# Optimization experiments

Hardware: AMD Instinct MI355X
Metric: run time of the kernel (lower is better)

The kernel has to match this reference:

```python
import jax, jax.numpy as jnp
import numpy as np

N, D_IN, H, C, K = 16384, 2048, 4096, 256, 256


def setup_inputs() -> dict:
    key = jax.random.key(0)
    ks = jax.random.split(key, 13)

    def lin(kw, kb, fan_in, fan_out):
        # torch Linear default init: U(-1/sqrt(fan_in), 1/sqrt(fan_in)); stored as [in, out]
        bound = 1.0 / np.sqrt(fan_in)
        W = jax.random.uniform(kw, (fan_in, fan_out), jnp.float32, -bound, bound)
        b = jax.random.uniform(kb, (fan_out,), jnp.float32, -bound, bound)
        return W, b

    W_e1, b_e1 = lin(ks[0], ks[1], D_IN, H)
    W_e2, b_e2 = lin(ks[2], ks[3], H, C)
    W_d1, b_d1 = lin(ks[4], ks[5], C, H)
    W_d2, b_d2 = lin(ks[6], ks[7], H, D_IN)
    # codebooks init U(-1/K, 1/K) per the torch code
    cb1 = jax.random.uniform(ks[8], (K, C), jnp.float32, -1.0 / K, 1.0 / K)
    cb2 = jax.random.uniform(ks[9], (K, C), jnp.float32, -1.0 / K, 1.0 / K)
    cb3 = jax.random.uniform(ks[10], (K, C), jnp.float32, -1.0 / K, 1.0 / K)
    x = jax.random.normal(ks[11], (N, D_IN), jnp.float32)
    return {"x": x, "W_e1": W_e1, "b_e1": b_e1, "W_e2": W_e2, "b_e2": b_e2,
            "cb1": cb1, "cb2": cb2, "cb3": cb3,
            "W_d1": W_d1, "b_d1": b_d1, "W_d2": W_d2, "b_d2": b_d2}


def _vq_stage(z, cb):
    # dist[n,k] = sum_c (cb[k,c] - z[n,c])^2 = ||z||^2 - 2 z.cb^T + ||cb||^2
    # (same math as the torch N x K x C broadcast, expressed as a GEMM)
    d = (jnp.sum(z * z, axis=1, keepdims=True)
         - 2.0 * (z @ cb.T)
         + jnp.sum(cb * cb, axis=1))            # [N, K]
    nearest = jnp.argmin(d, axis=1)             # [N]
    zq = cb[nearest]                            # gather [N, C]
    return nearest, zq


def reference(x, W_e1, b_e1, W_e2, b_e2, cb1, cb2, cb3, W_d1, b_d1, W_d2, b_d2):
    ze_1 = jax.nn.relu(x @ W_e1 + b_e1) @ W_e2 + b_e2     # [N, C]
    nearest_1, zq_1 = _vq_stage(ze_1, cb1)
    ze_2 = ze_1 - zq_1
    nearest_2, zq_2 = _vq_stage(ze_2, cb2)
    ze_3 = ze_2 - zq_2
    nearest_3, zq_3 = _vq_stage(ze_3, cb3)
    # straight-through estimator
    decoder_input = ze_1 + jax.lax.stop_gradient(zq_1 + zq_2 + zq_3 - ze_1)
    x_hat = jax.nn.sigmoid(decoder_input @ W_d1 + b_d1) @ W_d2 + b_d2
    return (x_hat, ze_1, ze_2, ze_3, zq_1, zq_2, zq_3, nearest_1, nearest_2, nearest_3)
```

## Files before the change

kernel.cpp:

```cpp
#include <hip/hip_runtime.h>
#include <cstddef>


#define NN 16384
#define DIN 2048
#define HH 4096
#define CC 256
#define QRED ((size_t)4096 * 256)
#define NZ 24

typedef unsigned short ushortT;
typedef __attribute__((ext_vector_type(8))) short bf16x8;
typedef __attribute__((ext_vector_type(4))) float f32x4;

__device__ __forceinline__ ushortT f2b(float v) {
    unsigned int u = __float_as_uint(v);
    return (ushortT)((u + 0x7fffu + ((u >> 16) & 1u)) >> 16);
}
__device__ __forceinline__ float b2f(ushortT s) {
    return __uint_as_float(((unsigned int)s) << 16);
}
__device__ __forceinline__ void split3(float v, ushortT& h, ushortT& m, ushortT& l) {
    h = f2b(v);
    float r1 = v - b2f(h);
    m = f2b(r1);
    l = f2b(r1 - b2f(m));
}

__device__ __forceinline__ void gld16(const void* g, void* l) {
    __builtin_amdgcn_global_load_lds(
        (const __attribute__((address_space(1))) unsigned int*)g,
        (__attribute__((address_space(3))) unsigned int*)l,
        16, 0, 0);
}

template<int NP>
__launch_bounds__(256)
__global__ void tsplit(const float* __restrict__ W,
                       ushortT* __restrict__ T0,
                       ushortT* __restrict__ T1,
                       ushortT* __restrict__ T2,
                       int K, int N)
{
    __shared__ float tile[32][33];
    const int k0 = blockIdx.y * 32, n0 = blockIdx.x * 32;
    const int c = threadIdx.x & 31, r = threadIdx.x >> 5;
    #pragma unroll
    for (int i = 0; i < 4; ++i)
        tile[r + 8*i][c] = W[(size_t)(k0 + r + 8*i) * N + n0 + c];
    __syncthreads();
    #pragma unroll
    for (int i = 0; i < 4; ++i) {
        const int nl = r + 8*i, kl = c;
        float v = tile[kl][nl];
        size_t o = (size_t)(n0 + nl) * K + k0 + kl;
        ushortT h = f2b(v);
        T0[o] = h;
        if (NP > 1) {
            float r1 = v - b2f(h);
            ushortT m = f2b(r1);
            T1[o] = m;
            T2[o] = f2b(r1 - b2f(m));
        }
    }
}

__launch_bounds__(256)
__global__ void split_src(const float* __restrict__ X,
                          ushortT* __restrict__ P0, ushortT* __restrict__ P1,
                          ushortT* __restrict__ P2, size_t n4)
{
    for (size_t i = (size_t)blockIdx.x * 256 + threadIdx.x; i < n4;
         i += (size_t)gridDim.x * 256) {
        float4 v = *(const float4*)(X + i * 4);
        ushort4 hv, mv, lv;
        split3(v.x, ((ushortT*)&hv)[0], ((ushortT*)&mv)[0], ((ushortT*)&lv)[0]);
        split3(v.y, ((ushortT*)&hv)[1], ((ushortT*)&mv)[1], ((ushortT*)&lv)[1]);
        split3(v.z, ((ushortT*)&hv)[2], ((ushortT*)&mv)[2], ((ushortT*)&lv)[2]);
        split3(v.w, ((ushortT*)&hv)[3], ((ushortT*)&mv)[3], ((ushortT*)&lv)[3]);
        *(ushort4*)(P0 + i * 4) = hv;
        *(ushort4*)(P1 + i * 4) = mv;
        *(ushort4*)(P2 + i * 4) = lv;
    }
}

template<int NSEG, int KSH, int NTC, int EPI, int OM>
__launch_bounds__(512, 2)
__global__ void gemm256(const ushortT* __restrict__ Ab, size_t aPl,
                        const ushortT* __restrict__ Bb, size_t bPl,
                        const float* __restrict__ bias,
                        float* __restrict__ Cf,
                        ushortT* __restrict__ Ob, size_t oPl,
                        int N, int K)
{
    __shared__ ushortT sh[65536];

    const int t    = threadIdx.x;
    const int lane = t & 63;
    const int wid  = t >> 6;
    const int l15  = lane & 15;
    const int l4   = lane >> 4;
    const int bm   = blockIdx.y * 256;
    const int bn   = blockIdx.x * 256;
    const int wm   = (wid >> 2) * 128;
    const int wn   = (wid & 3) * 64;
    const int t0   = (OM == 3) ? blockIdx.z * NTC : 0;

    constexpr unsigned PA_PACK = 0x210100u;
    constexpr unsigned PB_PACK = 0x012010u;

    const int trow = t >> 3;
    const unsigned tcol = (unsigned)(((t & 7) ^ (trow & 7)) * 8);
    unsigned gA[4], gB[4];
    #pragma unroll
    for (int i = 0; i < 4; ++i) {
        gA[i] = (unsigned)(bm + i * 64 + trow) * (unsigned)K + tcol;
        gB[i] = (unsigned)(bn + i * 64 + trow) * (unsigned)K + tcol;
    }
    const int ldsT = t * 8;

    auto stageH = [&](int buf, int gtt, int half) {
        const int seg = (NSEG > 1) ? (gtt >> KSH) : 0;
        const unsigned kin = ((unsigned)(gtt & ((1 << KSH) - 1))) << 6;
        const unsigned pa = (NSEG > 1) ? ((PA_PACK >> (seg * 4)) & 15u) : 0u;
        const unsigned pb = (NSEG > 1) ? ((PB_PACK >> (seg * 4)) & 15u) : 0u;
        const ushortT* Abase = Ab + (size_t)pa * aPl + kin;
        const ushortT* Bbase = Bb + (size_t)pb * bPl + kin;
        ushortT* lb = sh + buf * 32768;
        if (half == 0) {
            gld16(Abase + gA[0], lb + 0 * 4096 + ldsT);
            gld16(Abase + gA[2], lb + 2 * 4096 + ldsT);
            gld16(Bbase + gB[0], lb + 16384 + 0 * 4096 + ldsT);
            gld16(Bbase + gB[1], lb + 16384 + 1 * 4096 + ldsT);
        } else {
            gld16(Bbase + gB[2], lb + 16384 + 2 * 4096 + ldsT);
            gld16(Bbase + gB[3], lb + 16384 + 3 * 4096 + ldsT);
            gld16(Abase + gA[1], lb + 1 * 4096 + ldsT);
            gld16(Abase + gA[3], lb + 3 * 4096 + ldsT);
        }
    };

    f32x4 acc[8][4] = {};

    stageH(0, t0, 0);
    stageH(0, t0, 1);

    #pragma unroll 1
    for (int tt = 0; tt < NTC; ++tt) {
        const int buf = tt & 1;
        const ushortT* As = sh + buf * 32768;
        const ushortT* Bs = As + 16384;
        const bool notlast = (tt + 1 < NTC);
        bf16x8 a_[4], b_[4];

        asm volatile("s_waitcnt vmcnt(2)" ::: "memory");
        __builtin_amdgcn_sched_barrier(0);
        __builtin_amdgcn_s_barrier();
        __builtin_amdgcn_sched_barrier(0);
        #pragma unroll
        for (int ni = 0; ni < 4; ++ni) {
            const int rb = wn + ni * 16 + l15;
            b_[ni] = *(const bf16x8*)&Bs[rb * 64 + (l4 ^ (rb & 7)) * 8];
        }
        #pragma unroll
        for (int mi = 0; mi < 4; ++mi) {
            const int ra = wm + mi * 16 + l15;
            a_[mi] = *(const bf16x8*)&As[ra * 64 + (l4 ^ (ra & 7)) * 8];
        }
        if (notlast) stageH(buf ^ 1, t0 + tt + 1, 0);
        asm volatile("s_waitcnt lgkmcnt(0)" ::: "memory");
        __builtin_amdgcn_sched_barrier(0);
        __builtin_amdgcn_s_setprio(1);
        #pragma unroll
        for (int mi = 0; mi < 4; ++mi)
            #pragma unroll
            for (int ni = 0; ni < 4; ++ni)
                acc[mi][ni] = __builtin_amdgcn_mfma_f32_16x16x32_bf16(
                    a_[mi], b_[ni], acc[mi][ni], 0, 0, 0);
        __builtin_amdgcn_s_setprio(0);
        __builtin_amdgcn_sched_barrier(0);

        if (notlast) { asm volatile("s_waitcnt vmcnt(4)" ::: "memory"); }
        else         { asm volatile("s_waitcnt vmcnt(0)" ::: "memory"); }
        __builtin_amdgcn_sched_barrier(0);
        __builtin_amdgcn_s_barrier();
        __builtin_amdgcn_sched_barrier(0);
        #pragma unroll
        for (int mi = 0; mi < 4; ++mi) {
            const int ra = wm + (mi + 4) * 16 + l15;
            a_[mi] = *(const bf16x8*)&As[ra * 64 + (l4 ^ (ra & 7)) * 8];
        }
        if (notlast) stageH(buf ^ 1, t0 + tt + 1, 1);
        asm volatile("s_waitcnt lgkmcnt(0)" ::: "memory");
        __builtin_amdgcn_sched_barrier(0);
        __builtin_amdgcn_s_setprio(1);
        #pragma unroll
        for (int mi = 0; mi < 4; ++mi)
            #pragma unroll
            for (int ni = 0; ni < 4; ++ni)
                acc[mi + 4][ni] = __builtin_amdgcn_mfma_f32_16x16x32_bf16(
                    a_[mi], b_[ni], acc[mi + 4][ni], 0, 0, 0);
        __builtin_amdgcn_s_setprio(0);
        __builtin_amdgcn_sched_barrier(0);

        __builtin_amdgcn_s_barrier();
        __builtin_amdgcn_sched_barrier(0);
        #pragma unroll
        for (int ni = 0; ni < 4; ++ni) {
            const int rb = wn + ni * 16 + l15;
            b_[ni] = *(const bf16x8*)&Bs[rb * 64 + ((4 | l4) ^ (rb & 7)) * 8];
        }
        #pragma unroll
        for (int mi = 0; mi < 4; ++mi) {
            const int ra = wm + mi * 16 + l15;
            a_[mi] = *(const bf16x8*)&As[ra * 64 + ((4 | l4) ^ (ra & 7)) * 8];
        }
        asm volatile("s_waitcnt lgkmcnt(0)" ::: "memory");
        __builtin_amdgcn_sched_barrier(0);
        __builtin_amdgcn_s_setprio(1);
        #pragma unroll
        for (int mi = 0; mi < 4; ++mi)
            #pragma unroll
            for (int ni = 0; ni < 4; ++ni)
                acc[mi][ni] = __builtin_amdgcn_mfma_f32_16x16x32_bf16(
                    a_[mi], b_[ni], acc[mi][ni], 0, 0, 0);
        __builtin_amdgcn_s_setprio(0);
        __builtin_amdgcn_sched_barrier(0);

        __builtin_amdgcn_s_barrier();
        __builtin_amdgcn_sched_barrier(0);
        #pragma unroll
        for (int mi = 0; mi < 4; ++mi) {
            const int ra = wm + (mi + 4) * 16 + l15;
            a_[mi] = *(const bf16x8*)&As[ra * 64 + ((4 | l4) ^ (ra & 7)) * 8];
        }
        asm volatile("s_waitcnt lgkmcnt(0)" ::: "memory");
        __builtin_amdgcn_sched_barrier(0);
        __builtin_amdgcn_s_setprio(1);
        #pragma unroll
        for (int mi = 0; mi < 4; ++mi)
            #pragma unroll
            for (int ni = 0; ni < 4; ++ni)
                acc[mi + 4][ni] = __builtin_amdgcn_mfma_f32_16x16x32_bf16(
                    a_[mi], b_[ni], acc[mi + 4][ni], 0, 0, 0);
        __builtin_amdgcn_s_setprio(0);
        __builtin_amdgcn_sched_barrier(0);
    }

    #pragma unroll
    for (int ni = 0; ni < 4; ++ni) {
        const int gcol = bn + wn + ni * 16 + l15;
        float bvv = 0.0f;
        if (OM != 3) bvv = bias[gcol];
        #pragma unroll
        for (int mi = 0; mi < 8; ++mi) {
            #pragma unroll
            for (int r = 0; r < 4; ++r) {
                const int grow = bm + wm + mi * 16 + l4 * 4 + r;
                const size_t o = (size_t)grow * N + gcol;
                if (OM == 3) {
                    Cf[(size_t)blockIdx.z * oPl + o] = acc[mi][ni][r];
                } else {
                    float v = acc[mi][ni][r] + bvv;
                    if (EPI == 1) v = fmaxf(v, 0.0f);
                    if (EPI == 2) v = 1.0f / (1.0f + expf(-v));
                    if (OM == 0) {
                        Cf[o] = v;
                    } else if (OM == 2) {
                        Ob[o] = f2b(v);
                    } else {
                        ushortT hh, mm, ll;
                        split3(v, hh, mm, ll);
                        Ob[o] = hh; Ob[oPl + o] = mm; Ob[2 * oPl + o] = ll;
                    }
                }
            }
        }
    }
}

__launch_bounds__(256)
__global__ void reduce_z(const float* __restrict__ part,
                         const float* __restrict__ bias,
                         float* __restrict__ outp, int n4)
{
    const int i = blockIdx.x * 256 + threadIdx.x;
    if (i >= n4) return;
    float4 s = *(const float4*)(part + (size_t)i * 4);
    #pragma unroll
    for (int z = 1; z < NZ; ++z) {
        float4 p = *(const float4*)(part + (size_t)z * (QRED) + (size_t)i * 4);
        s.x = __fadd_rn(s.x, p.x); s.y = __fadd_rn(s.y, p.y);
        s.z = __fadd_rn(s.z, p.z); s.w = __fadd_rn(s.w, p.w);
    }
    const int c4 = (i * 4) & 255;
    float4 b = *(const float4*)(bias + c4);
    s.x = __fadd_rn(s.x, b.x); s.y = __fadd_rn(s.y, b.y);
    s.z = __fadd_rn(s.z, b.z); s.w = __fadd_rn(s.w, b.w);
    *(float4*)(outp + (size_t)i * 4) = s;
}

__launch_bounds__(256)
__global__ void vq_kernel(const float* __restrict__ ze1,
                          const float* __restrict__ cb1,
                          const float* __restrict__ cb2,
                          const float* __restrict__ cb3,
                          float* __restrict__ out_ze2, float* __restrict__ out_ze3,
                          float* __restrict__ out_zq1, float* __restrict__ out_zq2,
                          float* __restrict__ out_zq3,
                          float* __restrict__ out_n1,  float* __restrict__ out_n2,
                          float* __restrict__ out_n3,
                          ushortT* __restrict__ dec_p)
{
    __shared__ float Zs[16][260];
    __shared__ float Ds[16][260];
    __shared__ float DecS[16][260];
    __shared__ float Srow[16];
    __shared__ int   Kmin[16];

    const int t    = threadIdx.x;
    const int row0 = blockIdx.x * 16;

    for (int i = t; i < 16*64; i += 256) {
        int r = i >> 6, c4 = (i & 63) << 2;
        float4 v = *(const float4*)(ze1 + (size_t)(row0 + r) * 256 + c4);
        *(float4*)&Zs[r][c4] = v;
        float4 z = {0.f,0.f,0.f,0.f};
        *(float4*)&DecS[r][c4] = z;
    }
    __syncthreads();

    const float* cbs[3] = {cb1, cb2, cb3};
    float* zqs[3] = {out_zq1, out_zq2, out_zq3};
    float* nss[3] = {out_n1, out_n2, out_n3};

    for (int s = 0; s < 3; ++s) {
        const float* cb = cbs[s];
        if (t < 16) {
            float ssum = 0.f;
            for (int c = 0; c < 256; ++c) ssum = fmaf(Zs[t][c], Zs[t][c], ssum);
            Srow[t] = ssum;
        }
        __syncthreads();
        {
            float accr[16];
            #pragma unroll
            for (int r = 0; r < 16; ++r) accr[r] = 0.f;
            float c2 = 0.f;
            const float* cbrow = cb + (size_t)t * 256;
            for (int c4 = 0; c4 < 256; c4 += 4) {
                float4 cv = *(const float4*)(cbrow + c4);
                c2 = fmaf(cv.x,cv.x,fmaf(cv.y,cv.y,fmaf(cv.z,cv.z,fmaf(cv.w,cv.w,c2))));
                #pragma unroll
                for (int r = 0; r < 16; ++r) {
                    float4 zv = *(const float4*)&Zs[r][c4];
                    accr[r] = fmaf(zv.x,cv.x,fmaf(zv.y,cv.y,
                              fmaf(zv.z,cv.z,fmaf(zv.w,cv.w,accr[r]))));
                }
            }
            #pragma unroll
            for (int r = 0; r < 16; ++r) {
                float g2 = __fmul_rn(2.0f, accr[r]);
                float t1 = __fsub_rn(Srow[r], g2);
                Ds[r][t]  = __fadd_rn(t1, c2);
            }
        }
        __syncthreads();
        if (t < 16) {
            float best = Ds[t][0];
            int bk = 0;
            for (int k = 1; k < 256; ++k) {
                float v = Ds[t][k];
                if (v < best) { best = v; bk = k; }
            }
            Kmin[t] = bk;
            nss[s][row0 + t] = (float)bk;
        }
        __syncthreads();
        for (int i = t; i < 16*64; i += 256) {
            int r = i >> 6, c4 = (i & 63) << 2;
            const float* q = cb + (size_t)Kmin[r] * 256 + c4;
            float4 qv = *(const float4*)q;
            *(float4*)&zqs[s][(size_t)(row0 + r) * 256 + c4] = qv;
            float4 dv = *(float4*)&DecS[r][c4];
            dv.x = __fadd_rn(dv.x, qv.x); dv.y = __fadd_rn(dv.y, qv.y);
            dv.z = __fadd_rn(dv.z, qv.z); dv.w = __fadd_rn(dv.w, qv.w);
            *(float4*)&DecS[r][c4] = dv;
            if (s < 2) {
                float4 zv = *(float4*)&Zs[r][c4];
                zv.x = __fsub_rn(zv.x, qv.x); zv.y = __fsub_rn(zv.y, qv.y);
                zv.z = __fsub_rn(zv.z, qv.z); zv.w = __fsub_rn(zv.w, qv.w);
                *(float4*)&Zs[r][c4] = zv;
                float* oz = (s == 0) ? out_ze2 : out_ze3;
                *(float4*)&oz[(size_t)(row0 + r) * 256 + c4] = zv;
            }
        }
        __syncthreads();
    }

    for (int i = t; i < 16*64; i += 256) {
        int r = i >> 6, c4 = (i & 63) << 2;
        float4 z1 = *(const float4*)(ze1 + (size_t)(row0 + r) * 256 + c4);
        float4 dv = *(float4*)&DecS[r][c4];
        float4 o;
        o.x = __fadd_rn(z1.x, __fsub_rn(dv.x, z1.x));
        o.y = __fadd_rn(z1.y, __fsub_rn(dv.y, z1.y));
        o.z = __fadd_rn(z1.z, __fsub_rn(dv.z, z1.z));
        o.w = __fadd_rn(z1.w, __fsub_rn(dv.w, z1.w));
        ushort4 ov;
        ((ushortT*)&ov)[0] = f2b(o.x);
        ((ushortT*)&ov)[1] = f2b(o.y);
        ((ushortT*)&ov)[2] = f2b(o.z);
        ((ushortT*)&ov)[3] = f2b(o.w);
        *(ushort4*)(dec_p + (size_t)(row0 + r) * 256 + c4) = ov;
    }
}

extern "C" void kernel_launch(void* const* d_in, const int* in_sizes, int n_in,
                              void* d_out, int out_size, void* d_ws, size_t ws_size,
                              hipStream_t stream)
{
    const float* x   = (const float*)d_in[0];
    const float* We1 = (const float*)d_in[1];
    const float* be1 = (const float*)d_in[2];
    const float* We2 = (const float*)d_in[3];
    const float* be2 = (const float*)d_in[4];
    const float* cb1 = (const float*)d_in[5];
    const float* cb2 = (const float*)d_in[6];
    const float* cb3 = (const float*)d_in[7];
    const float* Wd1 = (const float*)d_in[8];
    const float* bd1 = (const float*)d_in[9];
    const float* Wd2 = (const float*)d_in[10];
    const float* bd2 = (const float*)d_in[11];

    float* out   = (float*)d_out;
    float* x_hat = out;
    float* ze1   = out + 33554432;
    float* ze2   = out + 37748736;
    float* ze3   = out + 41943040;
    float* zq1   = out + 46137344;
    float* zq2   = out + 50331648;
    float* zq3   = out + 54525952;
    float* n1    = out + 58720256;
    float* n2    = out + 58736640;
    float* n3    = out + 58753024;

    const int    QR   = 4096;
    const size_t szXq = (size_t)QR * DIN;
    const size_t szHq = (size_t)QR * HH;
    const size_t szW1 = (size_t)HH * DIN;
    const size_t szW2 = (size_t)CC * HH;

    ushortT* xq   = (ushortT*)d_ws;
    ushortT* hq   = xq + 3 * szXq;
    ushortT* We1t = hq + 3 * szHq;
    ushortT* We2t = We1t + 3 * szW1;
    ushortT* Wd1t = We2t + 3 * szW2;
    ushortT* Wd2t = Wd1t + szW2;
    ushortT* decp = Wd2t + szW1;
    float*   zpart = (float*)(decp + (size_t)NN * CC);
    ushortT* h2p  = xq;

    dim3 blk(256), blk5(512);

    tsplit<3><<<dim3(HH/32, DIN/32), blk, 0, stream>>>(We1, We1t, We1t+szW1, We1t+2*szW1, DIN, HH);
    tsplit<3><<<dim3(CC/32, HH/32),  blk, 0, stream>>>(We2, We2t, We2t+szW2, We2t+2*szW2, HH, CC);
    tsplit<1><<<dim3(HH/32, CC/32),  blk, 0, stream>>>(Wd1, Wd1t, nullptr, nullptr, CC, HH);
    tsplit<1><<<dim3(DIN/32, HH/32), blk, 0, stream>>>(Wd2, Wd2t, nullptr, nullptr, HH, DIN);

    for (int q = 0; q < 4; ++q) {
        split_src<<<dim3(2048), blk, 0, stream>>>(x + (size_t)q * szXq,
                                                  xq, xq + szXq, xq + 2*szXq, szXq / 4);
        gemm256<6,5,192,1,1><<<dim3(HH/256, QR/256), blk5, 0, stream>>>(
            xq, szXq, We1t, szW1, be1, nullptr, hq, szHq, HH, DIN);
        gemm256<6,6,16,0,3><<<dim3(CC/256, QR/256, NZ), blk5, 0, stream>>>(
            hq, szHq, We2t, szW2, nullptr, zpart, nullptr, QRED, CC, HH);
        reduce_z<<<dim3(QR*CC/4/256), blk, 0, stream>>>(
            zpart, be2, ze1 + (size_t)q * QR * CC, QR*CC/4);
    }

    vq_kernel<<<dim3(NN/16), blk, 0, stream>>>(ze1, cb1, cb2, cb3,
                                               ze2, ze3, zq1, zq2, zq3,
                                               n1, n2, n3, decp);

    gemm256<1,2,4,2,2><<<dim3(HH/256, NN/256), blk5, 0, stream>>>(
        decp, 0, Wd1t, 0, bd1, nullptr, h2p, 0, HH, CC);
    gemm256<1,6,64,0,0><<<dim3(DIN/256, NN/256), blk5, 0, stream>>>(
        h2p, 0, Wd2t, 0, bd2, x_hat, nullptr, 0, DIN, HH);
}
```

Before: 2.434 ms.

## Restructure GEMM main loop to one barrier per tile with register-prefetched fragments

Rewrites the inner K-loop of the bf16 MFMA GEMM. It waits for all global loads (vmcnt(0)) and uses a single barrier at the start of each tile, with a trailing barrier at the end, instead of four barriers per tile. LDS fragments for later MFMA groups are loaded ahead into separate register arrays so ds_reads overlap the preceding MFMAs, and the global stages for the next tile are issued between compute groups. The cost is more VGPRs for the extra fragment arrays, which could lower occupancy, and a full vmcnt(0) wait that may expose global-load latency.

Measured after the change: 2.421 ms. About the same (-0.5%).

```diff
diff --git a/kernel.cpp b/kernel.cpp
--- a/kernel.cpp
+++ b/kernel.cpp
@@ -151,99 +151,81 @@
         const ushortT* As = sh + buf * 32768;
         const ushortT* Bs = As + 16384;
         const bool notlast = (tt + 1 < NTC);
-        bf16x8 a_[4], b_[4];
-
-        asm volatile("s_waitcnt vmcnt(2)" ::: "memory");
+        bf16x8 b0[4], a0[4], a1[4], b1[4], a2[4], a3[4];
+
+        asm volatile("s_waitcnt vmcnt(0)" ::: "memory");
         __builtin_amdgcn_sched_barrier(0);
         __builtin_amdgcn_s_barrier();
         __builtin_amdgcn_sched_barrier(0);
+
         #pragma unroll
         for (int ni = 0; ni < 4; ++ni) {
             const int rb = wn + ni * 16 + l15;
-            b_[ni] = *(const bf16x8*)&Bs[rb * 64 + (l4 ^ (rb & 7)) * 8];
+            b0[ni] = *(const bf16x8*)&Bs[rb * 64 + (l4 ^ (rb & 7)) * 8];
         }
         #pragma unroll
         for (int mi = 0; mi < 4; ++mi) {
             const int ra = wm + mi * 16 + l15;
-            a_[mi] = *(const bf16x8*)&As[ra * 64 + (l4 ^ (ra & 7)) * 8];
-        }
-        if (notlast) stageH(buf ^ 1, t0 + tt + 1, 0);
-        asm volatile("s_waitcnt lgkmcnt(0)" ::: "memory");
-        __builtin_amdgcn_sched_barrier(0);
+            a0[mi] = *(const bf16x8*)&As[ra * 64 + (l4 ^ (ra & 7)) * 8];
+        }
+        #pragma unroll
+        for (int mi = 0; mi < 4; ++mi) {
+            const int ra = wm + (mi + 4) * 16 + l15;
+            a1[mi] = *(const bf16x8*)&As[ra * 64 + (l4 ^ (ra & 7)) * 8];
+        }
         __builtin_amdgcn_s_setprio(1);
         #pragma unroll
         for (int mi = 0; mi < 4; ++mi)
             #pragma unroll
             for (int ni = 0; ni < 4; ++ni)
                 acc[mi][ni] = __builtin_amdgcn_mfma_f32_16x16x32_bf16(
-                    a_[mi], b_[ni], acc[mi][ni], 0, 0, 0);
+                    a0[mi], b0[ni], acc[mi][ni], 0, 0, 0);
         __builtin_amdgcn_s_setprio(0);
         __builtin_amdgcn_sched_barrier(0);
-
-        if (notlast) { asm volatile("s_waitcnt vmcnt(4)" ::: "memory"); }
-        else         { asm volatile("s_waitcnt vmcnt(0)" ::: "memory"); }
-        __builtin_amdgcn_sched_barrier(0);
-        __builtin_amdgcn_s_barrier();
-        __builtin_amdgcn_sched_barrier(0);
+        if (notlast) stageH(buf ^ 1, t0 + tt + 1, 0);
+        #pragma unroll
+        for (int ni = 0; ni < 4; ++ni) {
+            const int rb = wn + ni * 16 + l15;
+            b1[ni] = *(const bf16x8*)&Bs[rb * 64 + ((4 | l4) ^ (rb & 7)) * 8];
+        }
+        #pragma unroll
+        for (int mi = 0; mi < 4; ++mi) {
+            const int ra = wm + mi * 16 + l15;
+            a2[mi] = *(const bf16x8*)&As[ra * 64 + ((4 | l4) ^ (ra & 7)) * 8];
+        }
+        __builtin_amdgcn_s_setprio(1);
+        #pragma unroll
+        for (int mi = 0; mi < 4; ++mi)
+            #pragma unroll
+            for (int ni = 0; ni < 4; ++ni)
+                acc[mi + 4][ni] = __builtin_amdgcn_mfma_f32_16x16x32_bf16(
+                    a1[mi], b0[ni], acc[mi + 4][ni], 0, 0, 0);
+        __builtin_amdgcn_s_setprio(0);
+        __builtin_amdgcn_sched_barrier(0);
+        if (notlast) stageH(buf ^ 1, t0 + tt + 1, 1);
         #pragma unroll
         for (int mi = 0; mi < 4; ++mi) {
             const int ra = wm + (mi + 4) * 16 + l15;
-            a_[mi] = *(const bf16x8*)&As[ra * 64 + (l4 ^ (ra & 7)) * 8];
-        }
-        if (notlast) stageH(buf ^ 1, t0 + tt + 1, 1);
-        asm volatile("s_waitcnt lgkmcnt(0)" ::: "memory");
-        __builtin_amdgcn_sched_barrier(0);
+            a3[mi] = *(const bf16x8*)&As[ra * 64 + ((4 | l4) ^ (ra & 7)) * 8];
+        }
+        __builtin_amdgcn_s_setprio(1);
+        #pragma unroll
+        for (int mi = 0; mi < 4; ++mi)
+            #pragma unroll
+            for (int ni = 0; ni < 4; ++ni)
+                acc[mi][ni] = __builtin_amdgcn_mfma_f32_16x16x32_bf16(
+                    a2[mi], b1[ni], acc[mi][ni], 0, 0, 0);
+        __builtin_amdgcn_s_setprio(0);
         __builtin_amdgcn_s_setprio(1);
         #pragma unroll
         for (int mi = 0; mi < 4; ++mi)
             #pragma unroll
             for (int ni = 0; ni < 4; ++ni)
                 acc[mi + 4][ni] = __builtin_amdgcn_mfma_f32_16x16x32_bf16(
-                    a_[mi], b_[ni], acc[mi + 4][ni], 0, 0, 0);
+                    a3[mi], b1[ni], acc[mi + 4][ni], 0, 0, 0);
         __builtin_amdgcn_s_setprio(0);
         __builtin_amdgcn_sched_barrier(0);
-
         __builtin_amdgcn_s_barrier();
-        __builtin_amdgcn_sched_barrier(0);
-        #pragma unroll
-        for (int ni = 0; ni < 4; ++ni) {
-            const int rb = wn + ni * 16 + l15;
-            b_[ni] = *(const bf16x8*)&Bs[rb * 64 + ((4 | l4) ^ (rb & 7)) * 8];
-        }
-        #pragma unroll
-        for (int mi = 0; mi < 4; ++mi) {
-            const int ra = wm + mi * 16 + l15;
-            a_[mi] = *(const bf16x8*)&As[ra * 64 + ((4 | l4) ^ (ra & 7)) * 8];
-        }
-        asm volatile("s_waitcnt lgkmcnt(0)" ::: "memory");
-        __builtin_amdgcn_sched_barrier(0);
-        __builtin_amdgcn_s_setprio(1);
-        #pragma unroll
-        for (int mi = 0; mi < 4; ++mi)
-            #pragma unroll
-            for (int ni = 0; ni < 4; ++ni)
-                acc[mi][ni] = __builtin_amdgcn_mfma_f32_16x16x32_bf16(
-                    a_[mi], b_[ni], acc[mi][ni], 0, 0, 0);
-        __builtin_amdgcn_s_setprio(0);
-        __builtin_amdgcn_sched_barrier(0);
-
-        __builtin_amdgcn_s_barrier();
-        __builtin_amdgcn_sched_barrier(0);
-        #pragma unroll
-        for (int mi = 0; mi < 4; ++mi) {
-            const int ra = wm + (mi + 4) * 16 + l15;
-            a_[mi] = *(const bf16x8*)&As[ra * 64 + ((4 | l4) ^ (ra & 7)) * 8];
-        }
-        asm volatile("s_waitcnt lgkmcnt(0)" ::: "memory");
-        __builtin_amdgcn_sched_barrier(0);
-        __builtin_amdgcn_s_setprio(1);
-        #pragma unroll
-        for (int mi = 0; mi < 4; ++mi)
-            #pragma unroll
-            for (int ni = 0; ni < 4; ++ni)
-                acc[mi + 4][ni] = __builtin_amdgcn_mfma_f32_16x16x32_bf16(
-                    a_[mi], b_[ni], acc[mi + 4][ni], 0, 0, 0);
-        __builtin_amdgcn_s_setprio(0);
         __builtin_amdgcn_sched_barrier(0);
     }
 
```
